# Optimization experiments

Measured on AMD Instinct MI355X. Metric: run time of the kernel, lower is better.

## Reference

```python
import jax, jax.numpy as jnp
import numpy as np

D_BINS = 16   # piecewise-linear bins
N_PROP = 10   # hard-coded in CountModule.__init__


def pwl(w, x):
    """PiecewiseLinear.forward: w is [D_BINS+1], x any shape in [0,1]."""
    aw = jnp.abs(w)
    nw = aw / aw.sum()
    cs = jnp.cumsum(nw)               # [17] cumulative knot values
    xd = x * D_BINS
    ip = jnp.floor(xd).astype(jnp.int32)   # x >= 0 so trunc == floor
    frac = xd - ip.astype(x.dtype)
    return cs[jnp.minimum(ip, D_BINS)] + frac * nw[jnp.minimum(ip + 1, D_BINS)]


def iou(a):
    """Pairwise IoU of boxes a [B,4,n] (coords y1,x1,y2,x2) -> [B,n,n]."""
    tl = jnp.maximum(a[:, :2, :, None], a[:, :2, None, :])  # [B,2,n,n]
    br = jnp.minimum(a[:, 2:, :, None], a[:, 2:, None, :])
    wh = jnp.clip(br - tl, 0.0)
    inter = wh[:, 0] * wh[:, 1]                               # [B,n,n]
    area = jnp.clip(a[:, 2] - a[:, 0], 0.0) * jnp.clip(a[:, 3] - a[:, 1], 0.0)  # [B,n]
    return inter / (area[:, :, None] + area[:, None, :] - inter + 1e-12)


def count_forward(boxes, attention, f_weights):
    n = N_PROP
    B = boxes.shape[0]
    f = lambda i, x: pwl(f_weights[i], x)
    # keep top-n proposals by attention score
    att_v, idx = jax.lax.top_k(attention, n)                  # [B,n]
    boxes_f = jnp.take_along_axis(
        boxes, jnp.broadcast_to(idx[:, None, :], (B, 4, n)), axis=2)  # [B,4,n]
    att = jax.nn.sigmoid(att_v)
    A = att[:, :, None] * att[:, None, :]                     # outer product [B,n,n]
    Dm = 1.0 - iou(boxes_f)                                   # [B,n,n]
    A_t = f(0, A) * f(1, Dm)
    X = f(3, A) * f(4, Dm)
    # deduplicate: outer_diff on 2D att gives pairwise |a_i - a_j|; on 3D X the
    # original torch code unsqueezes both operands at the same axis, yielding zeros
    att_diff = jnp.abs(att[:, :, None] - att[:, None, :])     # [B,n,n]
    xs = X[:, :, None, :]
    score_diff = jnp.broadcast_to(jnp.abs(xs - xs), (B, n, n, n))  # zeros, as in torch
    sim = f(2, 1.0 - att_diff) * jnp.prod(f(2, 1.0 - score_diff), axis=1)  # [B,n,n]
    s_i = sim.sum(axis=2)                                     # [B,n]
    s_st = s_i[:, :, None] * s_i[:, None, :]                  # [B,n,n]
    score = A_t / s_st
    corr = f(0, att * att) / s_i
    mod_E = score.sum(axis=(1, 2))[:, None] + corr.sum(axis=1, keepdims=True)  # [B,1]
    c = jnp.sqrt(mod_E + 1e-20)
    # to_k_hot: soft two-hot over counts 0..n
    cc = jnp.clip(c, 0.0, float(n))                           # [B,1]
    ip = jnp.floor(cc).astype(jnp.int32)
    frac = cc - ip.astype(cc.dtype)
    left = jax.nn.one_hot(jnp.minimum(ip[:, 0], n), n + 1, dtype=cc.dtype)
    right = jax.nn.one_hot(jnp.minimum(ip[:, 0] + 1, n), n + 1, dtype=cc.dtype)
    o = (1.0 - frac) * left + frac * right                    # [B,n+1]
    p_a = jnp.abs(f(5, att) - 0.5)                            # [B,n]
    p_d = jnp.abs(f(6, Dm) - 0.5)                             # [B,n,n]
    gate = f(7, p_a.mean(axis=1, keepdims=True)
             + p_d.mean(axis=2).mean(axis=1, keepdims=True))  # [B,1]
    return gate * o                                           # [B,n+1]


def setup_inputs() -> dict:
    key = jax.random.key(0)
    k1, k2, k3 = jax.random.split(key, 3)
    B, M = 32768, 36
    boxes = jax.random.uniform(k1, (B, 4, M), dtype=jnp.float32)
    attention = jax.random.normal(k2, (B, M), dtype=jnp.float32)
    f_weights = jax.random.uniform(k3, (8, D_BINS + 1), dtype=jnp.float32,
                                   minval=0.25, maxval=1.75)
    return {"boxes": boxes, "attention": attention, "f_weights": f_weights}


def reference(boxes, attention, f_weights):
    return count_forward(boxes, attention, f_weights)
```

## Files before the change

kernel.cpp:

```cpp
#include <hip/hip_runtime.h>
#include <cstdint>
#include <cstddef>

#define MM 36
#define NP 10

__device__ __forceinline__ float pwl_eval(const float2* __restrict__ Trow, float x) {
    float xd = x * 16.0f;
    float fip = floorf(xd);
    float frac = xd - fip;
    int ip = (int)fip;
    ip = ip < 0 ? 0 : (ip > 16 ? 16 : ip);
    float2 t = Trow[ip];
    return t.x + frac * t.y;
}

__global__ __launch_bounds__(64) void count_kernel(
    const float* __restrict__ boxes,
    const float* __restrict__ attention,
    const float* __restrict__ fw,
    float* __restrict__ out,
    int B)
{
    __shared__ float2 T[8][17];

    const int tid = threadIdx.x;
    const int b = blockIdx.x * 64 + tid;

    if (tid < 8) {
        const float* w = fw + tid * 17;
        float aw[17];
        float s = 0.f;
        #pragma unroll
        for (int k = 0; k < 17; ++k) { aw[k] = fabsf(w[k]); s += aw[k]; }
        float nw[17];
        #pragma unroll
        for (int k = 0; k < 17; ++k) nw[k] = aw[k] / s;
        float c = 0.f;
        #pragma unroll
        for (int k = 0; k < 17; ++k) {
            c += nw[k];
            T[tid][k] = make_float2(c, (k < 16) ? nw[k + 1] : nw[16]);
        }
    }

    float v[MM];
    if (b < B) {
        const float4* ap = reinterpret_cast<const float4*>(attention + (size_t)b * MM);
        #pragma unroll
        for (int q = 0; q < MM / 4; ++q) {
            float4 t = ap[q];
            v[q * 4 + 0] = t.x; v[q * 4 + 1] = t.y;
            v[q * 4 + 2] = t.z; v[q * 4 + 3] = t.w;
        }
    }
    __syncthreads();
    if (b >= B) return;

    unsigned long long selmask = 0ull;
    #pragma unroll
    for (int k = 0; k < NP; ++k) {
        float mx = -3.0e38f; int mi = 0;
        #pragma unroll
        for (int m = 0; m < MM; ++m) {
            bool avail = ((selmask >> m) & 1ull) == 0ull;
            bool better = avail && (v[m] > mx);
            mx = better ? v[m] : mx;
            mi = better ? m : mi;
        }
        selmask |= (1ull << mi);
    }
    unsigned long long packed = 0ull;
    int cnt = 0;
    #pragma unroll
    for (int m = 0; m < MM; ++m) {
        if ((selmask >> m) & 1ull) {
            packed |= ((unsigned long long)m) << (6 * cnt);
            ++cnt;
        }
    }

    const float* arow = attention + (size_t)b * MM;
    const float* brow = boxes + (size_t)b * (4 * MM);
    float satt[NP], y1[NP], x1[NP], y2[NP], x2[NP], area[NP];
    #pragma unroll
    for (int k = 0; k < NP; ++k) {
        int mk = (int)((packed >> (6 * k)) & 63ull);
        float av = arow[mk];
        satt[k] = 1.0f / (1.0f + __expf(-av));
        float a0 = brow[mk];
        float a1 = brow[mk + MM];
        float a2 = brow[mk + 2 * MM];
        float a3 = brow[mk + 3 * MM];
        y1[k] = a0; x1[k] = a1; y2[k] = a2; x2[k] = a3;
        area[k] = fmaxf(a2 - a0, 0.f) * fmaxf(a3 - a1, 0.f);
    }

    float cs2_16 = T[2][16].x;
    float p2 = cs2_16 * cs2_16;
    float p4 = p2 * p2;
    float p8 = p4 * p4;
    float P = p8 * p2;

    const float2* T0 = &T[0][0];
    const float2* T1 = &T[1][0];
    const float2* T2 = &T[2][0];
    const float2* T5 = &T[5][0];
    const float2* T6 = &T[6][0];
    const float2* T7 = &T[7][0];

    float s_row[NP];
    #pragma unroll
    for (int i = 0; i < NP; ++i) s_row[i] = 0.f;
    float at[NP * (NP + 1) / 2];
    float pd_sum = 0.f;

    #pragma unroll
    for (int i = 0; i < NP; ++i) {
        #pragma unroll
        for (int j = i; j < NP; ++j) {
            const int p = i * NP - (i * (i + 1)) / 2 + j;
            float ty = fmaxf(y1[i], y1[j]);
            float tx = fmaxf(x1[i], x1[j]);
            float by = fminf(y2[i], y2[j]);
            float bx = fminf(x2[i], x2[j]);
            float ih = fmaxf(by - ty, 0.f);
            float iw = fmaxf(bx - tx, 0.f);
            float inter = ih * iw;
            float iouv = __fdividef(inter, area[i] + area[j] - inter + 1e-12f);
            float Dm = fmaxf(1.0f - iouv, 0.0f);
            float A = satt[i] * satt[j];
            float a_t = pwl_eval(T0, A) * pwl_eval(T1, Dm);
            float simv = pwl_eval(T2, 1.0f - fabsf(satt[i] - satt[j])) * P;
            float pdv = fabsf(pwl_eval(T6, Dm) - 0.5f);
            at[p] = a_t;
            s_row[i] += simv;
            if (j > i) { s_row[j] += simv; pd_sum += 2.f * pdv; }
            else       { pd_sum += pdv; }
        }
    }

    float inv[NP];
    #pragma unroll
    for (int i = 0; i < NP; ++i) inv[i] = 1.0f / s_row[i];

    float score_sum = 0.f;
    #pragma unroll
    for (int i = 0; i < NP; ++i) {
        #pragma unroll
        for (int j = i; j < NP; ++j) {
            const int p = i * NP - (i * (i + 1)) / 2 + j;
            float sc = at[p] * inv[i] * inv[j];
            score_sum += (j > i) ? 2.f * sc : sc;
        }
    }

    float corr_sum = 0.f, pa_sum = 0.f;
    #pragma unroll
    for (int i = 0; i < NP; ++i) {
        corr_sum += pwl_eval(T0, satt[i] * satt[i]) * inv[i];
        pa_sum += fabsf(pwl_eval(T5, satt[i]) - 0.5f);
    }

    float gate = pwl_eval(T7, pa_sum * (1.0f / NP) + pd_sum * (1.0f / (NP * NP)));

    float mod_E = score_sum + corr_sum;
    float cval = sqrtf(mod_E + 1e-20f);
    cval = fminf(fmaxf(cval, 0.f), 10.0f);
    float fip = floorf(cval);
    int ipc = (int)fip;
    float frac = cval - fip;
    int i0 = ipc < 10 ? ipc : 10;
    int i1 = (ipc + 1) < 10 ? (ipc + 1) : 10;

    float* orow = out + (size_t)b * (NP + 1);
    #pragma unroll
    for (int k = 0; k <= NP; ++k) {
        float val = 0.f;
        val += (k == i0) ? (1.0f - frac) * gate : 0.f;
        val += (k == i1) ? frac * gate : 0.f;
        orow[k] = val;
    }
}

extern "C" void kernel_launch(void* const* d_in, const int* in_sizes, int n_in,
                              void* d_out, int out_size, void* d_ws, size_t ws_size,
                              hipStream_t stream) {
    const float* boxes = (const float*)d_in[0];
    const float* attention = (const float*)d_in[1];
    const float* fw = (const float*)d_in[2];
    float* out = (float*)d_out;
    int B = in_sizes[1] / MM;
    int grid = (B + 63) / 64;
    hipLaunchKernelGGL(count_kernel, dim3(grid), dim3(64), 0, stream,
                       boxes, attention, fw, out, B);
}
```

Baseline: 29.05 us.

## Split each batch row across 16 lanes with shuffle-based top-k and reductions

Work moves from one thread per batch row to a 16-lane group per row. Top-k becomes a wave shuffle max over packed value/index keys. Each lane computes one row of the pairwise IoU/PWL matrix, and the partial sums are combined with xor-shuffle reductions. Output writes become per-lane and coalesced. This cuts per-thread register pressure and serial work, and raises parallelism, at the cost of redundant box loads per lane, 6 of 16 lanes idling in the pairwise phase, and a full rather than symmetric pair matrix.

```diff
diff --git a/kernel.cpp b/kernel.cpp
--- a/kernel.cpp
+++ b/kernel.cpp
@@ -4,6 +4,7 @@
 
 #define MM 36
 #define NP 10
+#define BLOCK 256
 
 __device__ __forceinline__ float pwl_eval(const float2* __restrict__ Trow, float x) {
     float xd = x * 16.0f;
@@ -15,7 +16,17 @@
     return t.x + frac * t.y;
 }
 
-__global__ __launch_bounds__(64) void count_kernel(
+__device__ __forceinline__ unsigned long long umax64(unsigned long long a, unsigned long long b) {
+    return a > b ? a : b;
+}
+
+__device__ __forceinline__ unsigned long long pack_key(float v, int m) {
+    unsigned u = __float_as_uint(v);
+    u = ((int)u < 0) ? ~u : (u | 0x80000000u);
+    return ((unsigned long long)u << 32) | (unsigned)(63 - m);
+}
+
+__global__ __launch_bounds__(BLOCK, 4) void count_kernel(
     const float* __restrict__ boxes,
     const float* __restrict__ attention,
     const float* __restrict__ fw,
@@ -25,7 +36,6 @@
     __shared__ float2 T[8][17];
 
     const int tid = threadIdx.x;
-    const int b = blockIdx.x * 64 + tid;
 
     if (tid < 8) {
         const float* w = fw + tid * 17;
@@ -43,57 +53,48 @@
             T[tid][k] = make_float2(c, (k < 16) ? nw[k + 1] : nw[16]);
         }
     }
+    __syncthreads();
 
-    float v[MM];
-    if (b < B) {
-        const float4* ap = reinterpret_cast<const float4*>(attention + (size_t)b * MM);
-        #pragma unroll
-        for (int q = 0; q < MM / 4; ++q) {
-            float4 t = ap[q];
-            v[q * 4 + 0] = t.x; v[q * 4 + 1] = t.y;
-            v[q * 4 + 2] = t.z; v[q * 4 + 3] = t.w;
-        }
-    }
-    __syncthreads();
+    const int lane = tid & 63;
+    const int l    = lane & 15;
+    const int b    = blockIdx.x * (BLOCK / 16) + (tid >> 4);
     if (b >= B) return;
-
-    unsigned long long selmask = 0ull;
-    #pragma unroll
-    for (int k = 0; k < NP; ++k) {
-        float mx = -3.0e38f; int mi = 0;
-        #pragma unroll
-        for (int m = 0; m < MM; ++m) {
-            bool avail = ((selmask >> m) & 1ull) == 0ull;
-            bool better = avail && (v[m] > mx);
-            mx = better ? v[m] : mx;
-            mi = better ? m : mi;
-        }
-        selmask |= (1ull << mi);
-    }
-    unsigned long long packed = 0ull;
-    int cnt = 0;
-    #pragma unroll
-    for (int m = 0; m < MM; ++m) {
-        if ((selmask >> m) & 1ull) {
-            packed |= ((unsigned long long)m) << (6 * cnt);
-            ++cnt;
-        }
-    }
 
     const float* arow = attention + (size_t)b * MM;
     const float* brow = boxes + (size_t)b * (4 * MM);
-    float satt[NP], y1[NP], x1[NP], y2[NP], x2[NP], area[NP];
+
+    unsigned long long k0 = pack_key(arow[l], l);
+    unsigned long long k1 = pack_key(arow[l + 16], l + 16);
+    unsigned long long k2 = (l < 4) ? pack_key(arow[l + 32], l + 32) : 0ull;
+
+    unsigned long long packed = 0ull;
     #pragma unroll
-    for (int k = 0; k < NP; ++k) {
-        int mk = (int)((packed >> (6 * k)) & 63ull);
-        float av = arow[mk];
-        satt[k] = 1.0f / (1.0f + __expf(-av));
-        float a0 = brow[mk];
-        float a1 = brow[mk + MM];
-        float a2 = brow[mk + 2 * MM];
-        float a3 = brow[mk + 3 * MM];
-        y1[k] = a0; x1[k] = a1; y2[k] = a2; x2[k] = a3;
-        area[k] = fmaxf(a2 - a0, 0.f) * fmaxf(a3 - a1, 0.f);
+    for (int t = 0; t < NP; ++t) {
+        unsigned long long km = umax64(umax64(k0, k1), k2);
+        km = umax64(km, __shfl_xor(km, 1));
+        km = umax64(km, __shfl_xor(km, 2));
+        km = umax64(km, __shfl_xor(km, 4));
+        km = umax64(km, __shfl_xor(km, 8));
+        int mt = 63 - (int)(km & 63ull);
+        packed |= ((unsigned long long)mt) << (6 * t);
+        k0 = (mt == l)      ? 0ull : k0;
+        k1 = (mt == l + 16) ? 0ull : k1;
+        k2 = (mt == l + 32) ? 0ull : k2;
+    }
+
+    float satt[NP], y1[NP], x1[NP], y2[NP], x2[NP], area[NP], at[NP];
+    #pragma unroll
+    for (int t = 0; t < NP; ++t) {
+        int m = (int)((packed >> (6 * t)) & 63ull);
+        float av = arow[m];
+        satt[t] = 1.0f / (1.0f + __expf(-av));
+        float a0 = brow[m];
+        float a1 = brow[m + MM];
+        float a2 = brow[m + 2 * MM];
+        float a3 = brow[m + 3 * MM];
+        y1[t] = a0; x1[t] = a1; y2[t] = a2; x2[t] = a3;
+        area[t] = fmaxf(a2 - a0, 0.f) * fmaxf(a3 - a1, 0.f);
+        at[t] = 0.f;
     }
 
     float cs2_16 = T[2][16].x;
@@ -109,63 +110,58 @@
     const float2* T6 = &T[6][0];
     const float2* T7 = &T[7][0];
 
-    float s_row[NP];
-    #pragma unroll
-    for (int i = 0; i < NP; ++i) s_row[i] = 0.f;
-    float at[NP * (NP + 1) / 2];
-    float pd_sum = 0.f;
+    float s_i = 0.f, pd_i = 0.f, pa_i = 0.f;
+    float sattI = 0.f;
+    if (l < NP) {
+        int mo = (int)((packed >> (6 * l)) & 63ull);
+        float av = arow[mo];
+        sattI = 1.0f / (1.0f + __expf(-av));
+        float y1I = brow[mo];
+        float x1I = brow[mo + MM];
+        float y2I = brow[mo + 2 * MM];
+        float x2I = brow[mo + 3 * MM];
+        float areaI = fmaxf(y2I - y1I, 0.f) * fmaxf(x2I - x1I, 0.f);
 
-    #pragma unroll
-    for (int i = 0; i < NP; ++i) {
         #pragma unroll
-        for (int j = i; j < NP; ++j) {
-            const int p = i * NP - (i * (i + 1)) / 2 + j;
-            float ty = fmaxf(y1[i], y1[j]);
-            float tx = fmaxf(x1[i], x1[j]);
-            float by = fminf(y2[i], y2[j]);
-            float bx = fminf(x2[i], x2[j]);
+        for (int j = 0; j < NP; ++j) {
+            float ty = fmaxf(y1I, y1[j]);
+            float tx = fmaxf(x1I, x1[j]);
+            float by = fminf(y2I, y2[j]);
+            float bx = fminf(x2I, x2[j]);
             float ih = fmaxf(by - ty, 0.f);
             float iw = fmaxf(bx - tx, 0.f);
             float inter = ih * iw;
-            float iouv = __fdividef(inter, area[i] + area[j] - inter + 1e-12f);
+            float iouv = __fdividef(inter, areaI + area[j] - inter + 1e-12f);
             float Dm = fmaxf(1.0f - iouv, 0.0f);
-            float A = satt[i] * satt[j];
-            float a_t = pwl_eval(T0, A) * pwl_eval(T1, Dm);
-            float simv = pwl_eval(T2, 1.0f - fabsf(satt[i] - satt[j])) * P;
-            float pdv = fabsf(pwl_eval(T6, Dm) - 0.5f);
-            at[p] = a_t;
-            s_row[i] += simv;
-            if (j > i) { s_row[j] += simv; pd_sum += 2.f * pdv; }
-            else       { pd_sum += pdv; }
+            float A = sattI * satt[j];
+            at[j] = pwl_eval(T0, A) * pwl_eval(T1, Dm);
+            s_i += pwl_eval(T2, 1.0f - fabsf(sattI - satt[j])) * P;
+            pd_i += fabsf(pwl_eval(T6, Dm) - 0.5f);
         }
+        pa_i = fabsf(pwl_eval(T5, sattI) - 0.5f);
     }
 
-    float inv[NP];
+    float inv_i = 1.0f / s_i;
+    const int gbase = lane & 48;
+    float dot = 0.f;
     #pragma unroll
-    for (int i = 0; i < NP; ++i) inv[i] = 1.0f / s_row[i];
+    for (int j = 0; j < NP; ++j) {
+        float ivj = __shfl(inv_i, gbase + j);
+        dot = fmaf(at[j], ivj, dot);
+    }
+    float score_i = inv_i * dot;
+    float corr_i = pwl_eval(T0, sattI * sattI) * inv_i;
+    float contrib = (l < NP) ? (score_i + corr_i) : 0.f;
 
-    float score_sum = 0.f;
     #pragma unroll
-    for (int i = 0; i < NP; ++i) {
-        #pragma unroll
-        for (int j = i; j < NP; ++j) {
-            const int p = i * NP - (i * (i + 1)) / 2 + j;
-            float sc = at[p] * inv[i] * inv[j];
-            score_sum += (j > i) ? 2.f * sc : sc;
-        }
+    for (int s = 1; s < 16; s <<= 1) {
+        contrib += __shfl_xor(contrib, s);
+        pa_i    += __shfl_xor(pa_i, s);
+        pd_i    += __shfl_xor(pd_i, s);
     }
 
-    float corr_sum = 0.f, pa_sum = 0.f;
-    #pragma unroll
-    for (int i = 0; i < NP; ++i) {
-        corr_sum += pwl_eval(T0, satt[i] * satt[i]) * inv[i];
-        pa_sum += fabsf(pwl_eval(T5, satt[i]) - 0.5f);
-    }
-
-    float gate = pwl_eval(T7, pa_sum * (1.0f / NP) + pd_sum * (1.0f / (NP * NP)));
-
-    float mod_E = score_sum + corr_sum;
-    float cval = sqrtf(mod_E + 1e-20f);
+    float gate = pwl_eval(T7, pa_i * 0.1f + pd_i * 0.01f);
+    float cval = sqrtf(contrib + 1e-20f);
     cval = fminf(fmaxf(cval, 0.f), 10.0f);
     float fip = floorf(cval);
     int ipc = (int)fip;
@@ -173,13 +169,10 @@
     int i0 = ipc < 10 ? ipc : 10;
     int i1 = (ipc + 1) < 10 ? (ipc + 1) : 10;
 
-    float* orow = out + (size_t)b * (NP + 1);
-    #pragma unroll
-    for (int k = 0; k <= NP; ++k) {
-        float val = 0.f;
-        val += (k == i0) ? (1.0f - frac) * gate : 0.f;
-        val += (k == i1) ? frac * gate : 0.f;
-        orow[k] = val;
+    if (l < NP + 1) {
+        float val = ((l == i0) ? (1.0f - frac) * gate : 0.f)
+                  + ((l == i1) ? frac * gate : 0.f);
+        out[(size_t)b * (NP + 1) + l] = val;
     }
 }
 
@@ -191,7 +184,8 @@
     const float* fw = (const float*)d_in[2];
     float* out = (float*)d_out;
     int B = in_sizes[1] / MM;
-    int grid = (B + 63) / 64;
-    hipLaunchKernelGGL(count_kernel, dim3(grid), dim3(64), 0, stream,
+    int batches_per_block = BLOCK / 16;
+    int grid = (B + batches_per_block - 1) / batches_per_block;
+    hipLaunchKernelGGL(count_kernel, dim3(grid), dim3(BLOCK), 0, stream,
                        boxes, attention, fw, out, B);
 }
```

Measured after the change: 28.73 us. About the same (-1.1%).
